# Kernel optimization log

Measured on AMD Instinct MI355X. Metric: run time of the kernel, lower is better.

The kernel has to match this reference:

```python
import jax, jax.numpy as jnp
import numpy as np

N_ATOM = 10000
N_EDGE = 40000
D = 64          # fingerprint_dim
BOND_DIM = 10
EPS_BN = 1e-6
EPS_SM = 1e-8


def _bn(x, g, b, m, v):
    # BatchNorm1d in eval mode with running stats
    return (x - m) * jax.lax.rsqrt(v + EPS_BN) * g + b


def setup_inputs() -> dict:
    key = jax.random.key(0)
    ks = jax.random.split(key, 16)
    s = 0.05
    inp = {
        "atom": jax.random.normal(ks[0], (N_ATOM, D), jnp.float32),
        "bond_index": jax.random.randint(ks[1], (N_EDGE, 2), 0, N_ATOM, jnp.int64),
        "bond": jax.random.normal(ks[2], (N_EDGE, BOND_DIM), jnp.float32),
        # encoder: Linear(bond_dim, D*D) + BN(D*D)
        "enc_W": jax.random.normal(ks[3], (D * D, BOND_DIM), jnp.float32) * s,
        "enc_b": jnp.zeros((D * D,), jnp.float32),
        "bn1_g": jnp.ones((D * D,), jnp.float32),
        "bn1_b": jnp.zeros((D * D,), jnp.float32),
        "bn1_m": jnp.zeros((D * D,), jnp.float32),
        "bn1_v": jnp.ones((D * D,), jnp.float32),
        # align: Linear(2D, 1)
        "align_W": jax.random.normal(ks[4], (1, 2 * D), jnp.float32) * s,
        "align_b": jnp.zeros((1,), jnp.float32),
        # attend: Linear(D, D) + BN(D)
        "att_W": jax.random.normal(ks[5], (D, D), jnp.float32) * s,
        "att_b": jnp.zeros((D,), jnp.float32),
        "bn2_g": jnp.ones((D,), jnp.float32),
        "bn2_b": jnp.zeros((D,), jnp.float32),
        "bn2_m": jnp.zeros((D,), jnp.float32),
        "bn2_v": jnp.ones((D,), jnp.float32),
        # GRUCell(D, D)
        "gru_Wih": jax.random.normal(ks[6], (3 * D, D), jnp.float32) * s,
        "gru_Whh": jax.random.normal(ks[7], (3 * D, D), jnp.float32) * s,
        "gru_bih": jnp.zeros((3 * D,), jnp.float32),
        "gru_bhh": jnp.zeros((3 * D,), jnp.float32),
    }
    return inp


def reference(atom, bond_index, bond, enc_W, enc_b, bn1_g, bn1_b, bn1_m, bn1_v,
              align_W, align_b, att_W, att_b, bn2_g, bn2_b, bn2_m, bn2_v,
              gru_Wih, gru_Whh, gru_bih, gru_bhh):
    num_atom, atom_dim = atom.shape
    tgt = bond_index[:, 0]  # segment index (bond_index.t()[0])
    nbr = bond_index[:, 1]

    # encoder: Linear + BN + ReLU, then view as per-edge [D, D] matrices
    enc = jax.nn.relu(_bn(bond @ enc_W.T + enc_b, bn1_g, bn1_b, bn1_m, bn1_v))
    enc = enc.reshape(-1, atom_dim, atom_dim)            # [E, D, D]

    neighbor = jnp.einsum('ed,edf->ef', atom[nbr], enc)  # per-edge bmm [E, D]
    target_atom = atom[tgt]

    feat = jnp.concatenate([target_atom, neighbor], axis=-1)       # [E, 2D]
    align_score = jax.nn.leaky_relu(feat @ align_W.T + align_b)    # [E, 1]

    atend = _bn(neighbor @ att_W.T + att_b, bn2_g, bn2_b, bn2_m, bn2_v)  # [E, D]

    # segment softmax over edges grouped by target atom
    seg_max = jax.ops.segment_max(align_score, tgt, num_segments=num_atom)
    ex = jnp.exp(align_score - seg_max[tgt])
    denom = jax.ops.segment_sum(ex, tgt, num_segments=num_atom)[tgt] + EPS_SM
    w = ex / denom                                                   # [E, 1]

    context = jax.ops.segment_sum(w * atend, tgt, num_segments=num_atom)  # [N, D]
    context = jax.nn.elu(context)

    # GRUCell(context, atom)
    gi = context @ gru_Wih.T + gru_bih
    gh = atom @ gru_Whh.T + gru_bhh
    i_r, i_z, i_n = jnp.split(gi, 3, axis=-1)
    h_r, h_z, h_n = jnp.split(gh, 3, axis=-1)
    r = jax.nn.sigmoid(i_r + h_r)
    z = jax.nn.sigmoid(i_z + h_z)
    n = jnp.tanh(i_n + r * h_n)
    update = (1.0 - z) * n + z * atom
    return update
```

## Files before the change

### kernel.cpp

```cpp
#include <hip/hip_runtime.h>

#define N_ATOM 10000
#define N_EDGE 40000
#define DD 64
#define BOND_DIM 10
#define EPS_BN 1e-6f
#define EPS_SM 1e-8f
#define GA 8

typedef __attribute__((ext_vector_type(8))) short short8;
typedef __attribute__((ext_vector_type(4))) float float4v;
typedef __attribute__((ext_vector_type(16))) float float16v;
typedef unsigned int u32;

constexpr size_t OFF_AFRAG   = 0;
constexpr size_t OFF_ATTFRAG = 32768;
constexpr size_t OFF_ATTB    = 34816;
constexpr size_t OFF_WIHT    = 34880;
constexpr size_t OFF_WHHT    = 47168;
constexpr size_t OFF_DENOM   = 59456;
constexpr size_t OFF_CTX     = 69456;

__device__ __forceinline__ unsigned short f2bf(float x) {
    u32 u = __float_as_uint(x);
    u32 r = u + 0x7FFFu + ((u >> 16) & 1u);
    return (unsigned short)(r >> 16);
}

__global__ void fold_kernel(const float* enc_W, const float* enc_b,
                            const float* g1, const float* b1,
                            const float* m1, const float* v1,
                            const float* att_W, const float* att_b,
                            const float* g2, const float* b2v,
                            const float* m2, const float* v2,
                            const float* Wih, const float* Whh,
                            float* ws) {
    u32* wsu = (u32*)ws;
    size_t i = (size_t)blockIdx.x * 256 + threadIdx.x;
    if (i < 8192) {
        int d = i >> 7, rem = i & 127;
        int ch = rem >> 6, l = rem & 63;
        int c = d * 64 + ch * 32 + (l & 31);
        int kb = 8 * (l >> 5);
        float s = g1[c] * rsqrtf(v1[c] + EPS_BN);
        float bias = enc_b[c] * s + b1[c] - m1[c] * s;
        unsigned short h[8];
#pragma unroll
        for (int j = 0; j < 8; j++) {
            int k = kb + j;
            float v = (k < BOND_DIM) ? enc_W[c * BOND_DIM + k] * s
                                     : ((k == BOND_DIM) ? bias : 0.f);
            h[j] = f2bf(v);
        }
#pragma unroll
        for (int m = 0; m < 4; m++)
            wsu[OFF_AFRAG + i * 4 + m] = (u32)h[2 * m] | ((u32)h[2 * m + 1] << 16);
    } else if (i < 8704) {
        int idx = i - 8192;
        int l = idx & 63, fckh = idx >> 6;
        int fc = fckh >> 1, kh = fckh & 1, q = l >> 4;
        int n = (fc << 4) + (l & 15);
        float s = g2[n] * rsqrtf(v2[n] + EPS_BN);
        unsigned short h[8];
#pragma unroll
        for (int j = 0; j < 8; j++) {
            int k = 32 * kh + 8 * q + j;
            h[j] = f2bf(att_W[n * DD + k] * s);
        }
#pragma unroll
        for (int m = 0; m < 4; m++)
            wsu[OFF_ATTFRAG + (size_t)idx * 4 + m] = (u32)h[2 * m] | ((u32)h[2 * m + 1] << 16);
    } else if (i < 8768) {
        int f = i - 8704;
        float s = g2[f] * rsqrtf(v2[f] + EPS_BN);
        ws[OFF_ATTB + f] = att_b[f] * s + b2v[f] - m2[f] * s;
    } else if (i < 21056) {
        int j = i - 8768;
        int d = j / 192, t = j % 192;
        ws[OFF_WIHT + j] = Wih[t * DD + d];
    } else if (i < 33344) {
        int j = i - 21056;
        int d = j / 192, t = j % 192;
        ws[OFF_WHHT + j] = Whh[t * DD + d];
    } else {
        size_t z = i - 33344;
        if (z < (size_t)N_ATOM + (size_t)N_ATOM * DD) ws[OFF_DENOM + z] = 0.f;
    }
}

__global__ __launch_bounds__(128) void edge_kernel(
    const float* atom, const int* bidx, const float* bond,
    const float* alignW, const float* alignb,
    const float* ws, float* denom, float* ctx) {
    __shared__ float s_bond[32][BOND_DIM];
    __shared__ float s_anbr[32][65];
    __shared__ float s_nbp[2][32][65];
    __shared__ float s_ex[32];
    __shared__ int   s_tgt[32];

    const int t = threadIdx.x;
    const int lane = t & 63;
    const int h = t >> 6;
    const int e0 = blockIdx.x * 32;

    for (int idx = t; idx < 32 * BOND_DIM; idx += 128)
        s_bond[idx / BOND_DIM][idx % BOND_DIM] = bond[(size_t)e0 * BOND_DIM + idx];
    if (t < 32) s_tgt[t] = bidx[2 * (e0 + t)];
    for (int e = h; e < 32; e += 2) {
        int nbr = bidx[2 * (e0 + e) + 1];
        s_anbr[e][lane] = atom[(size_t)nbr * DD + lane];
    }
    __syncthreads();

    const int eb = lane & 31;
    const int kb = 8 * (lane >> 5);
    short8 bfrag;
#pragma unroll
    for (int j = 0; j < 8; j++) {
        int k = kb + j;
        unsigned short hh = 0;
        if (k < BOND_DIM) hh = f2bf(s_bond[eb][k]);
        else if (k == BOND_DIM) hh = 0x3F80u;
        bfrag[j] = (short)hh;
    }

    const short8* afrag = (const short8*)((const u32*)ws + OFF_AFRAG);
    float16v zero16 = {};
    float nb0[16] = {}, nb1[16] = {};
    const int d0 = 32 * h;

    short8 a0 = afrag[(size_t)(d0 * 2 + 0) * 64 + lane];
    short8 a1 = afrag[(size_t)(d0 * 2 + 1) * 64 + lane];
#pragma unroll 2
    for (int it = 0; it < 32; it++) {
        int d = d0 + it;
        short8 n0, n1;
        if (it < 31) {
            n0 = afrag[(size_t)((d + 1) * 2 + 0) * 64 + lane];
            n1 = afrag[(size_t)((d + 1) * 2 + 1) * 64 + lane];
        }
        float av = s_anbr[eb][d];
        float16v enc0 = __builtin_amdgcn_mfma_f32_32x32x16_bf16(a0, bfrag, zero16, 0, 0, 0);
        float16v enc1 = __builtin_amdgcn_mfma_f32_32x32x16_bf16(a1, bfrag, zero16, 0, 0, 0);
#pragma unroll
        for (int r = 0; r < 16; r++) {
            nb0[r] = fmaf(av, fmaxf(enc0[r], 0.f), nb0[r]);
            nb1[r] = fmaf(av, fmaxf(enc1[r], 0.f), nb1[r]);
        }
        a0 = n0; a1 = n1;
    }

    const int fro = 4 * (lane >> 5);
#pragma unroll
    for (int r = 0; r < 16; r++) {
        int f = (r & 3) + 8 * (r >> 2) + fro;
        s_nbp[h][eb][f] = nb0[r];
        s_nbp[h][eb][32 + f] = nb1[r];
    }
    __syncthreads();

    const int es = h * 16;
    const int q = lane >> 4;
    const int r16 = lane & 15;

    short8 na[2];
#pragma unroll
    for (int kh = 0; kh < 2; kh++)
#pragma unroll
        for (int j = 0; j < 8; j++) {
            int k = 32 * kh + 8 * q + j;
            na[kh][j] = (short)f2bf(s_nbp[0][es + r16][k] + s_nbp[1][es + r16][k]);
        }
    const short8* battfrag = (const short8*)((const u32*)ws + OFF_ATTFRAG);
    const float4v zero4 = {0.f, 0.f, 0.f, 0.f};
    float4v att[4];
#pragma unroll
    for (int fc = 0; fc < 4; fc++) {
        att[fc] = __builtin_amdgcn_mfma_f32_16x16x32_bf16(na[0], battfrag[(fc * 2 + 0) * 64 + lane], zero4, 0, 0, 0);
        att[fc] = __builtin_amdgcn_mfma_f32_16x16x32_bf16(na[1], battfrag[(fc * 2 + 1) * 64 + lane], att[fc], 0, 0, 0);
        float ab = ws[OFF_ATTB + fc * 16 + r16];
#pragma unroll
        for (int r = 0; r < 4; r++) att[fc][r] += ab;
    }

    const float aw1 = alignW[lane];
    const float aw2 = alignW[64 + lane];
    const float alb = alignb[0];
#pragma unroll 4
    for (int e = 0; e < 16; e++) {
        int le = es + e;
        int tgt = s_tgt[le];
        float nbv = s_nbp[0][le][lane] + s_nbp[1][le][lane];
        float v = atom[(size_t)tgt * DD + lane] * aw1 + nbv * aw2;
#pragma unroll
        for (int off = 32; off > 0; off >>= 1) v += __shfl_xor(v, off);
        float sc = v + alb;
        sc = sc > 0.f ? sc : 0.01f * sc;
        float ex = expf(sc);
        if (lane == 0) {
            s_ex[le] = ex;
            atomicAdd(&denom[tgt], ex);
        }
    }

#pragma unroll
    for (int r = 0; r < 4; r++) {
        int le = es + 4 * q + r;
        float exr = s_ex[le];
        int tg = s_tgt[le];
#pragma unroll
        for (int fc = 0; fc < 4; fc++)
            atomicAdd(&ctx[(size_t)tg * DD + fc * 16 + r16], exr * att[fc][r]);
    }
}

__global__ __launch_bounds__(192) void gru_kernel(
    const float* atom, const float* ws, const float* denom, const float* ctx,
    const float* bih, const float* bhh, float* out) {
    __shared__ float sctx[GA][DD];
    __shared__ float satom[GA][DD];
    __shared__ float sgi[GA][192];
    __shared__ float sgh[GA][192];
    const int a0 = blockIdx.x * GA;
    const int t = threadIdx.x;

    for (int idx = t; idx < GA * DD; idx += 192) {
        int a = idx >> 6, f = idx & 63;
        float c = ctx[(size_t)(a0 + a) * DD + f] / (denom[a0 + a] + EPS_SM);
        sctx[a][f] = c > 0.f ? c : expm1f(c);
        satom[a][f] = atom[(size_t)(a0 + a) * DD + f];
    }
    __syncthreads();

    const float* wiht = ws + OFF_WIHT;
    const float* whht = ws + OFF_WHHT;
    float gi[GA], gh[GA];
    const float bi = bih[t], bh = bhh[t];
#pragma unroll
    for (int a = 0; a < GA; a++) { gi[a] = bi; gh[a] = bh; }
#pragma unroll 4
    for (int d = 0; d < DD; d++) {
        float wi = wiht[d * 192 + t];
        float wh = whht[d * 192 + t];
#pragma unroll
        for (int a = 0; a < GA; a++) {
            gi[a] = fmaf(wi, sctx[a][d], gi[a]);
            gh[a] = fmaf(wh, satom[a][d], gh[a]);
        }
    }
#pragma unroll
    for (int a = 0; a < GA; a++) { sgi[a][t] = gi[a]; sgh[a][t] = gh[a]; }
    __syncthreads();

    for (int idx = t; idx < GA * DD; idx += 192) {
        int a = idx >> 6, f = idx & 63;
        float r = 1.f / (1.f + expf(-(sgi[a][f] + sgh[a][f])));
        float z = 1.f / (1.f + expf(-(sgi[a][64 + f] + sgh[a][64 + f])));
        float n = tanhf(sgi[a][128 + f] + r * sgh[a][128 + f]);
        out[(size_t)(a0 + a) * DD + f] = (1.f - z) * n + z * satom[a][f];
    }
}

extern "C" void kernel_launch(void* const* d_in, const int* in_sizes, int n_in,
                              void* d_out, int out_size, void* d_ws, size_t ws_size,
                              hipStream_t stream) {
    const float* atom   = (const float*)d_in[0];
    const int*   bidx   = (const int*)d_in[1];
    const float* bond   = (const float*)d_in[2];
    const float* enc_W  = (const float*)d_in[3];
    const float* enc_b  = (const float*)d_in[4];
    const float* bn1_g  = (const float*)d_in[5];
    const float* bn1_b  = (const float*)d_in[6];
    const float* bn1_m  = (const float*)d_in[7];
    const float* bn1_v  = (const float*)d_in[8];
    const float* alignW = (const float*)d_in[9];
    const float* alignb = (const float*)d_in[10];
    const float* att_W  = (const float*)d_in[11];
    const float* att_b  = (const float*)d_in[12];
    const float* bn2_g  = (const float*)d_in[13];
    const float* bn2_b  = (const float*)d_in[14];
    const float* bn2_m  = (const float*)d_in[15];
    const float* bn2_v  = (const float*)d_in[16];
    const float* gWih   = (const float*)d_in[17];
    const float* gWhh   = (const float*)d_in[18];
    const float* gbih   = (const float*)d_in[19];
    const float* gbhh   = (const float*)d_in[20];

    float* ws  = (float*)d_ws;
    float* out = (float*)d_out;

    fold_kernel<<<2670, 256, 0, stream>>>(enc_W, enc_b, bn1_g, bn1_b, bn1_m, bn1_v,
                                          att_W, att_b, bn2_g, bn2_b, bn2_m, bn2_v,
                                          gWih, gWhh, ws);

    edge_kernel<<<N_EDGE / 32, 128, 0, stream>>>(
        atom, bidx, bond, alignW, alignb, ws,
        ws + OFF_DENOM, ws + OFF_CTX);

    gru_kernel<<<N_ATOM / GA, 192, 0, stream>>>(atom, ws, ws + OFF_DENOM, ws + OFF_CTX,
                                                gbih, gbhh, out);
}
```

Before: 164.5 us.

## Split edge kernel across four waves with staggered fragment order and role specialization

The edge kernel now runs 256 threads per block, so each of four waves handles 16 of the 64 input dimensions instead of 32. Partial neighbor sums are combined in shared memory over two barriers. Each block also starts its loop over the encoder weight fragments at a rotated offset, which spreads which fragments are read at the same time. After the combine, two waves compute the attend projection while the other two compute the alignment scores and denominators, and an added barrier is needed before the context atomics. The aim is more latency hiding and overlap, paid for with extra barriers, a shared-memory read-modify-write pass and higher register pressure under the launch bound.

```diff
diff --git a/kernel.cpp b/kernel.cpp
--- a/kernel.cpp
+++ b/kernel.cpp
@@ -88,7 +88,7 @@
     }
 }
 
-__global__ __launch_bounds__(128) void edge_kernel(
+__global__ __launch_bounds__(256, 5) void edge_kernel(
     const float* atom, const int* bidx, const float* bond,
     const float* alignW, const float* alignb,
     const float* ws, float* denom, float* ctx) {
@@ -103,10 +103,10 @@
     const int h = t >> 6;
     const int e0 = blockIdx.x * 32;
 
-    for (int idx = t; idx < 32 * BOND_DIM; idx += 128)
+    for (int idx = t; idx < 32 * BOND_DIM; idx += 256)
         s_bond[idx / BOND_DIM][idx % BOND_DIM] = bond[(size_t)e0 * BOND_DIM + idx];
     if (t < 32) s_tgt[t] = bidx[2 * (e0 + t)];
-    for (int e = h; e < 32; e += 2) {
+    for (int e = h; e < 32; e += 4) {
         int nbr = bidx[2 * (e0 + e) + 1];
         s_anbr[e][lane] = atom[(size_t)nbr * DD + lane];
     }
@@ -127,19 +127,21 @@
     const short8* afrag = (const short8*)((const u32*)ws + OFF_AFRAG);
     float16v zero16 = {};
     float nb0[16] = {}, nb1[16] = {};
-    const int d0 = 32 * h;
-
-    short8 a0 = afrag[(size_t)(d0 * 2 + 0) * 64 + lane];
-    short8 a1 = afrag[(size_t)(d0 * 2 + 1) * 64 + lane];
+    const int d0 = 16 * h;
+    const int ph = blockIdx.x & 15;
+
+    int dcur = d0 + (ph & 15);
+    short8 a0 = afrag[(size_t)(dcur * 2 + 0) * 64 + lane];
+    short8 a1 = afrag[(size_t)(dcur * 2 + 1) * 64 + lane];
 #pragma unroll 2
-    for (int it = 0; it < 32; it++) {
-        int d = d0 + it;
+    for (int it = 0; it < 16; it++) {
+        int dnxt = d0 + ((it + 1 + ph) & 15);
         short8 n0, n1;
-        if (it < 31) {
-            n0 = afrag[(size_t)((d + 1) * 2 + 0) * 64 + lane];
-            n1 = afrag[(size_t)((d + 1) * 2 + 1) * 64 + lane];
-        }
-        float av = s_anbr[eb][d];
+        if (it < 15) {
+            n0 = afrag[(size_t)(dnxt * 2 + 0) * 64 + lane];
+            n1 = afrag[(size_t)(dnxt * 2 + 1) * 64 + lane];
+        }
+        float av = s_anbr[eb][dcur];
         float16v enc0 = __builtin_amdgcn_mfma_f32_32x32x16_bf16(a0, bfrag, zero16, 0, 0, 0);
         float16v enc1 = __builtin_amdgcn_mfma_f32_32x32x16_bf16(a1, bfrag, zero16, 0, 0, 0);
 #pragma unroll
@@ -147,70 +149,86 @@
             nb0[r] = fmaf(av, fmaxf(enc0[r], 0.f), nb0[r]);
             nb1[r] = fmaf(av, fmaxf(enc1[r], 0.f), nb1[r]);
         }
-        a0 = n0; a1 = n1;
+        a0 = n0; a1 = n1; dcur = dnxt;
     }
 
     const int fro = 4 * (lane >> 5);
-#pragma unroll
-    for (int r = 0; r < 16; r++) {
-        int f = (r & 3) + 8 * (r >> 2) + fro;
-        s_nbp[h][eb][f] = nb0[r];
-        s_nbp[h][eb][32 + f] = nb1[r];
-    }
-    __syncthreads();
-
-    const int es = h * 16;
+    if (h < 2) {
+#pragma unroll
+        for (int r = 0; r < 16; r++) {
+            int f = (r & 3) + 8 * (r >> 2) + fro;
+            s_nbp[h][eb][f] = nb0[r];
+            s_nbp[h][eb][32 + f] = nb1[r];
+        }
+    }
+    __syncthreads();
+    if (h >= 2) {
+#pragma unroll
+        for (int r = 0; r < 16; r++) {
+            int f = (r & 3) + 8 * (r >> 2) + fro;
+            s_nbp[h - 2][eb][f] += nb0[r];
+            s_nbp[h - 2][eb][32 + f] += nb1[r];
+        }
+    }
+    __syncthreads();
+
+    const int es = (h & 1) * 16;
     const int q = lane >> 4;
     const int r16 = lane & 15;
-
-    short8 na[2];
-#pragma unroll
-    for (int kh = 0; kh < 2; kh++)
-#pragma unroll
-        for (int j = 0; j < 8; j++) {
-            int k = 32 * kh + 8 * q + j;
-            na[kh][j] = (short)f2bf(s_nbp[0][es + r16][k] + s_nbp[1][es + r16][k]);
-        }
-    const short8* battfrag = (const short8*)((const u32*)ws + OFF_ATTFRAG);
-    const float4v zero4 = {0.f, 0.f, 0.f, 0.f};
     float4v att[4];
-#pragma unroll
-    for (int fc = 0; fc < 4; fc++) {
-        att[fc] = __builtin_amdgcn_mfma_f32_16x16x32_bf16(na[0], battfrag[(fc * 2 + 0) * 64 + lane], zero4, 0, 0, 0);
-        att[fc] = __builtin_amdgcn_mfma_f32_16x16x32_bf16(na[1], battfrag[(fc * 2 + 1) * 64 + lane], att[fc], 0, 0, 0);
-        float ab = ws[OFF_ATTB + fc * 16 + r16];
-#pragma unroll
-        for (int r = 0; r < 4; r++) att[fc][r] += ab;
-    }
-
-    const float aw1 = alignW[lane];
-    const float aw2 = alignW[64 + lane];
-    const float alb = alignb[0];
+
+    if (h < 2) {
+        short8 na[2];
+#pragma unroll
+        for (int kh = 0; kh < 2; kh++)
+#pragma unroll
+            for (int j = 0; j < 8; j++) {
+                int k = 32 * kh + 8 * q + j;
+                na[kh][j] = (short)f2bf(s_nbp[0][es + r16][k] + s_nbp[1][es + r16][k]);
+            }
+        const short8* battfrag = (const short8*)((const u32*)ws + OFF_ATTFRAG);
+        const float4v zero4 = {0.f, 0.f, 0.f, 0.f};
+#pragma unroll
+        for (int fc = 0; fc < 4; fc++) {
+            att[fc] = __builtin_amdgcn_mfma_f32_16x16x32_bf16(na[0], battfrag[(fc * 2 + 0) * 64 + lane], zero4, 0, 0, 0);
+            att[fc] = __builtin_amdgcn_mfma_f32_16x16x32_bf16(na[1], battfrag[(fc * 2 + 1) * 64 + lane], att[fc], 0, 0, 0);
+            float ab = ws[OFF_ATTB + fc * 16 + r16];
+#pragma unroll
+            for (int r = 0; r < 4; r++) att[fc][r] += ab;
+        }
+    } else {
+        const float aw1 = alignW[lane];
+        const float aw2 = alignW[64 + lane];
+        const float alb = alignb[0];
 #pragma unroll 4
-    for (int e = 0; e < 16; e++) {
-        int le = es + e;
-        int tgt = s_tgt[le];
-        float nbv = s_nbp[0][le][lane] + s_nbp[1][le][lane];
-        float v = atom[(size_t)tgt * DD + lane] * aw1 + nbv * aw2;
-#pragma unroll
-        for (int off = 32; off > 0; off >>= 1) v += __shfl_xor(v, off);
-        float sc = v + alb;
-        sc = sc > 0.f ? sc : 0.01f * sc;
-        float ex = expf(sc);
-        if (lane == 0) {
-            s_ex[le] = ex;
-            atomicAdd(&denom[tgt], ex);
-        }
-    }
-
-#pragma unroll
-    for (int r = 0; r < 4; r++) {
-        int le = es + 4 * q + r;
-        float exr = s_ex[le];
-        int tg = s_tgt[le];
-#pragma unroll
-        for (int fc = 0; fc < 4; fc++)
-            atomicAdd(&ctx[(size_t)tg * DD + fc * 16 + r16], exr * att[fc][r]);
+        for (int e = 0; e < 16; e++) {
+            int le = es + e;
+            int tgt = s_tgt[le];
+            float nbv = s_nbp[0][le][lane] + s_nbp[1][le][lane];
+            float v = atom[(size_t)tgt * DD + lane] * aw1 + nbv * aw2;
+#pragma unroll
+            for (int off = 32; off > 0; off >>= 1) v += __shfl_xor(v, off);
+            float sc = v + alb;
+            sc = sc > 0.f ? sc : 0.01f * sc;
+            float ex = expf(sc);
+            if (lane == 0) {
+                s_ex[le] = ex;
+                atomicAdd(&denom[tgt], ex);
+            }
+        }
+    }
+    __syncthreads();
+
+    if (h < 2) {
+#pragma unroll
+        for (int r = 0; r < 4; r++) {
+            int le = es + 4 * q + r;
+            float exr = s_ex[le];
+            int tg = s_tgt[le];
+#pragma unroll
+            for (int fc = 0; fc < 4; fc++)
+                atomicAdd(&ctx[(size_t)tg * DD + fc * 16 + r16], exr * att[fc][r]);
+        }
     }
 }
 
@@ -293,7 +311,7 @@
                                           att_W, att_b, bn2_g, bn2_b, bn2_m, bn2_v,
                                           gWih, gWhh, ws);
 
-    edge_kernel<<<N_EDGE / 32, 128, 0, stream>>>(
+    edge_kernel<<<N_EDGE / 32, 256, 0, stream>>>(
         atom, bidx, bond, alignW, alignb, ws,
         ws + OFF_DENOM, ws + OFF_CTX);
 
```

New measurement: 149.0 us. 9.4% less time.
